# Kernel tuning notes

Measured on AMD Instinct MI355X. Metric: run time of the kernel, lower is better.

## Reference

```python
import jax, jax.numpy as jnp
import numpy as np

K_NN = 32          # configs['k']
LEAKY_ALPHA = 0.2  # configs['alpha']
NHEADS = 8         # all heads share gat_W0/gat_a0 in the weights dict -> tiled output
NEG_INF = -9e15    # masked-softmax fill used by dense GAT


@jax.custom_vjp
def grad_reverse(x):
    # GradientReversalLayer: identity forward, negated gradient backward
    return x

def _gr_fwd(x):
    return x, None

def _gr_bwd(res, g):
    return (-g,)

grad_reverse.defvjp(_gr_fwd, _gr_bwd)


def setup_inputs() -> dict:
    key = jax.random.key(0)
    ks = jax.random.split(key, 11)
    N, D = 6144, 512           # N = (num_domains+1)*batch_size = 4*1536
    H1, H2, G = 256, 128, 64   # hidden_layers=[256,128], gat_hidden=[64]
    C, ND = 16, 3              # num_classes, num source-domain discriminators

    def xav(k, shape):
        limit = np.float32(np.sqrt(6.0 / (shape[0] + shape[1])) * 1.414)
        return jax.random.uniform(k, shape, jnp.float32, -limit, limit)

    return {
        "x": jax.random.normal(ks[0], (N, D), jnp.float32),
        "fc_W0": xav(ks[1], (D, H1)),
        "fc_b0": jax.random.normal(ks[2], (H1,), jnp.float32) * 0.01,
        "fc_W1": xav(ks[3], (H1, H2)),
        "fc_b1": jax.random.normal(ks[4], (H2,), jnp.float32) * 0.01,
        "gat_W": xav(ks[5], (H2, G)),
        "gat_a": jax.random.normal(ks[6], (2 * G, 1), jnp.float32) * 0.1,
        "cls_W": xav(ks[7], (NHEADS * G, C)),
        "cls_b": jax.random.normal(ks[8], (C,), jnp.float32) * 0.01,
        "dsc_W": jax.random.uniform(ks[9], (ND, NHEADS * G, 2), jnp.float32),
        "dsc_b": jax.random.uniform(ks[10], (ND, 2), jnp.float32),
    }


def reference(x, fc_W0, fc_b0, fc_W1, fc_b1, gat_W, gat_a, cls_W, cls_b, dsc_W, dsc_b):
    # --- feature extractor MLP (Linear 'fc' + relu), dropout=0 / eval mode ---
    h = jax.nn.relu(x @ fc_W0 + fc_b0)
    h = jax.nn.relu(h @ fc_W1 + fc_b1)          # [N, 128]
    n = h.shape[0]

    # --- AdjacencyLayer / DistanceLayer: kNN over pairwise L2 distances ---
    sq = jnp.sum(h * h, axis=1)
    d2 = sq[:, None] + sq[None, :] - 2.0 * (h @ h.T)      # [N, N] squared dists
    d2 = d2 + jnp.eye(n, dtype=h.dtype) * 1e9             # exclude self from kNN
    _, idx = jax.lax.top_k(-jax.lax.stop_gradient(d2), K_NN)  # [N, K]
    adj = jnp.zeros((n, n), h.dtype).at[jnp.arange(n)[:, None], idx].set(1.0)
    adj = adj + jnp.eye(n, dtype=h.dtype)                 # self loops

    # --- dense GraphAttentionLayer (single shared head, tiled nheads times) ---
    Wh = h @ gat_W                                        # [N, G]
    Gd = Wh.shape[1]
    f1 = Wh @ gat_a[:Gd]                                  # [N, 1]
    f2 = Wh @ gat_a[Gd:]                                  # [N, 1]
    e = jax.nn.leaky_relu(f1 + f2.T, LEAKY_ALPHA)         # [N, N]
    att = jax.nn.softmax(jnp.where(adj > 0, e, NEG_INF), axis=1)
    hp = jax.nn.elu(att @ Wh)                             # [N, G]
    gat_out = jnp.tile(hp, (1, NHEADS))                   # concat of shared heads

    # --- class head + domain discriminators behind gradient reversal ---
    cls_logits = gat_out @ cls_W + cls_b                  # [N, C]
    rev = grad_reverse(gat_out)
    dsc_logits = jnp.einsum('nd,kdo->nko', rev, dsc_W) + dsc_b  # [N, ND, 2]
    return jnp.concatenate([cls_logits, dsc_logits.reshape(n, -1)], axis=1)
```

## Files before the change

kernel.cpp:

```cpp
#include <hip/hip_runtime.h>
#include <float.h>

#define N_PTS 6144
#define D_IN  512
#define H1_DIM 256
#define H2_DIM 128
#define G_DIM  64
#define KNN    32
#define NOUT   22

typedef short s8v __attribute__((ext_vector_type(8)));
typedef float f32x4 __attribute__((ext_vector_type(4)));
typedef unsigned u32x4 __attribute__((ext_vector_type(4)));
typedef unsigned short u16;
typedef unsigned long long u64;

__device__ __forceinline__ u16 f2bf(float f) {
  unsigned u = __float_as_uint(f);
  u += 0x7FFFu + ((u >> 16) & 1u);
  return (u16)(u >> 16);
}
__device__ __forceinline__ float bf2f(u16 s) {
  return __uint_as_float(((unsigned)s) << 16);
}
__device__ __forceinline__ void split3(float v, u16& a0, u16& a1, u16& a2) {
  a0 = f2bf(v);
  float r1 = v - bf2f(a0);
  a1 = f2bf(r1);
  a2 = f2bf(r1 - bf2f(a1));
}
__device__ __forceinline__ unsigned sortkey(float f) {
  unsigned ub = __float_as_uint(f);
  return (ub & 0x80000000u) ? ~ub : (ub | 0x80000000u);
}

template<int BM, bool AF32, bool SPLITK, bool BIAS, bool RELU, bool WF32, bool WSPLIT, bool WKEY, bool SYMM>
__global__ __launch_bounds__(256, 4) void mfma_gemm(
    const void* __restrict__ A0any, const u16* __restrict__ A1_, const u16* __restrict__ A2_,
    const u16* __restrict__ B0_, const u16* __restrict__ B1_, const u16* __restrict__ B2_,
    const float* __restrict__ bias,
    float* __restrict__ Cf, u16* __restrict__ C0, u16* __restrict__ C1, u16* __restrict__ C2,
    int Ktot, int Ks, int ldC, size_t MN, int rowoff)
{
  if (SYMM) {
    if ((int)(blockIdx.x >> 1) < (int)blockIdx.y) return;
  }
  const int MT = BM / 32, NT = 2;
  const int APL = BM * 32;
  const int BBASE = 3 * APL;
  __shared__ u16 lds[(BM + 64) * 32 * 3];

  const int t = threadIdx.x;
  const int lane = t & 63, wave = t >> 6;
  const int wm = wave >> 1, wn = wave & 1;
  const int m0 = blockIdx.y * BM, n0 = blockIdx.x * 64;
  const int kz = blockIdx.z * Ks;

  f32x4 acc[MT][NT] = {};

  const int pA = BM / 16;
  const int NC = 3 * pA + 12;

  for (int k0 = 0; k0 < Ks; k0 += 32) {
    if (k0) __syncthreads();
    const int kb = kz + k0;
    if (AF32) {
      const float* A = (const float*)A0any;
      #pragma unroll
      for (int c0 = 0; c0 < BM * 4; c0 += 256) {
        int c = c0 + t;
        int row = c >> 2, slot = c & 3;
        const float* g = A + (size_t)(m0 + row) * Ktot + kb + slot * 8;
        f32x4 fa = *(const f32x4*)g;
        f32x4 fb = *(const f32x4*)(g + 4);
        int dst = row * 32 + ((slot ^ ((row >> 1) & 3)) << 3);
        s8v v0, v1, v2;
        #pragma unroll
        for (int e = 0; e < 4; ++e) {
          u16 a0, a1, a2; split3(fa[e], a0, a1, a2);
          v0[e] = (short)a0; v1[e] = (short)a1; v2[e] = (short)a2;
        }
        #pragma unroll
        for (int e = 0; e < 4; ++e) {
          u16 a0, a1, a2; split3(fb[e], a0, a1, a2);
          v0[4 + e] = (short)a0; v1[4 + e] = (short)a1; v2[4 + e] = (short)a2;
        }
        *(s8v*)(lds + dst) = v0;
        *(s8v*)(lds + APL + dst) = v1;
        *(s8v*)(lds + 2 * APL + dst) = v2;
      }
      for (int c = wave; c < 12; c += 4) {
        int p = c >> 2, lc = c & 3;
        int row = lc * 16 + (lane >> 2);
        int srcslot = (lane & 3) ^ ((row >> 1) & 3);
        const u16* src = (p == 0) ? B0_ : (p == 1) ? B1_ : B2_;
        const u16* g = src + (size_t)(n0 + row) * Ktot + kb + srcslot * 8;
        __builtin_amdgcn_global_load_lds(
            (const __attribute__((address_space(1))) unsigned*)g,
            (__attribute__((address_space(3))) unsigned*)(lds + BBASE + p * 2048 + lc * 512),
            16, 0, 0);
      }
    } else {
      for (int c = wave; c < NC; c += 4) {
        const u16* src; int dstoff; int row0; int lc;
        if (c < 3 * pA) {
          int p = c / pA; lc = c % pA;
          src = (p == 0) ? (const u16*)A0any : (p == 1) ? A1_ : A2_;
          dstoff = p * APL + lc * 512;
          row0 = m0;
        } else {
          int cb = c - 3 * pA;
          int p = cb >> 2; lc = cb & 3;
          src = (p == 0) ? B0_ : (p == 1) ? B1_ : B2_;
          dstoff = BBASE + p * 2048 + lc * 512;
          row0 = n0;
        }
        int row = lc * 16 + (lane >> 2);
        int srcslot = (lane & 3) ^ ((row >> 1) & 3);
        const u16* g = src + (size_t)(row0 + row) * Ktot + kb + srcslot * 8;
        __builtin_amdgcn_global_load_lds(
            (const __attribute__((address_space(1))) unsigned*)g,
            (__attribute__((address_space(3))) unsigned*)(lds + dstoff),
            16, 0, 0);
      }
    }
    __syncthreads();

    s8v af[3][MT], bf[3][NT];
    #pragma unroll
    for (int mt = 0; mt < MT; ++mt) {
      int r = wm * (BM / 2) + mt * 16 + (lane & 15);
      int off = r * 32 + (((lane >> 4) ^ ((r >> 1) & 3)) << 3);
      #pragma unroll
      for (int p = 0; p < 3; ++p) af[p][mt] = *(const s8v*)(lds + p * APL + off);
    }
    #pragma unroll
    for (int nt = 0; nt < NT; ++nt) {
      int r = wn * 32 + nt * 16 + (lane & 15);
      int off = r * 32 + (((lane >> 4) ^ ((r >> 1) & 3)) << 3);
      #pragma unroll
      for (int p = 0; p < 3; ++p) bf[p][nt] = *(const s8v*)(lds + BBASE + p * 2048 + off);
    }
    #pragma unroll
    for (int mt = 0; mt < MT; ++mt)
      #pragma unroll
      for (int nt = 0; nt < NT; ++nt) {
        f32x4 a = acc[mt][nt];
        a = __builtin_amdgcn_mfma_f32_16x16x32_bf16(af[0][mt], bf[0][nt], a, 0, 0, 0);
        a = __builtin_amdgcn_mfma_f32_16x16x32_bf16(af[0][mt], bf[1][nt], a, 0, 0, 0);
        a = __builtin_amdgcn_mfma_f32_16x16x32_bf16(af[1][mt], bf[0][nt], a, 0, 0, 0);
        a = __builtin_amdgcn_mfma_f32_16x16x32_bf16(af[1][mt], bf[1][nt], a, 0, 0, 0);
        a = __builtin_amdgcn_mfma_f32_16x16x32_bf16(af[0][mt], bf[2][nt], a, 0, 0, 0);
        a = __builtin_amdgcn_mfma_f32_16x16x32_bf16(af[2][mt], bf[0][nt], a, 0, 0, 0);
        acc[mt][nt] = a;
      }
  }

  const bool mirror = SYMM && ((int)(blockIdx.x >> 1) > (int)blockIdx.y);
  unsigned* ldsT = (unsigned*)lds;

  #pragma unroll
  for (int mt = 0; mt < MT; ++mt) {
    #pragma unroll
    for (int nt = 0; nt < NT; ++nt) {
      int col = n0 + wn * 32 + nt * 16 + (lane & 15);
      float bv = (BIAS && !SPLITK) ? bias[col] : 0.f;
      float sqc = WKEY ? bias[col] : 0.f;
      #pragma unroll
      for (int v = 0; v < 4; ++v) {
        int row = m0 + wm * (BM / 2) + mt * 16 + (lane >> 4) * 4 + v;
        float val = acc[mt][nt][v] + bv;
        size_t o = (size_t)row * ldC + col;
        if (SPLITK) {
          Cf[(size_t)blockIdx.z * MN + o] = val;
        } else if (WKEY) {
          float f = fmaf(-2.f, val, sqc);
          unsigned uu = sortkey(f);
          if (rowoff + row == col) uu = 0xFFFFFFFFu;
          ((unsigned*)Cf)[o] = uu;
          if (mirror) {
            float fb2 = fmaf(-2.f, val, bias[row]);
            acc[mt][nt][v] = __uint_as_float(sortkey(fb2));
          }
        } else {
          if (RELU) val = fmaxf(val, 0.f);
          if (WF32) Cf[o] = val;
          if (WSPLIT) {
            u16 a0, a1, a2; split3(val, a0, a1, a2);
            C0[o] = a0; C1[o] = a1; C2[o] = a2;
          }
        }
      }
    }
  }

  if (WKEY && mirror) {
    __syncthreads();
    #pragma unroll
    for (int mt = 0; mt < MT; ++mt) {
      #pragma unroll
      for (int nt = 0; nt < NT; ++nt) {
        int cl = wn * 32 + nt * 16 + (lane & 15);
        #pragma unroll
        for (int v = 0; v < 4; ++v) {
          int rl = wm * (BM / 2) + mt * 16 + (lane >> 4) * 4 + v;
          ldsT[cl * 129 + rl] = __float_as_uint(acc[mt][nt][v]);
        }
      }
    }
    __syncthreads();
    unsigned* Cu = (unsigned*)Cf;
    for (int e = t; e < 64 * 32; e += 256) {
      int jr = e >> 5, cq = e & 31;
      u32x4 vv;
      #pragma unroll
      for (int x = 0; x < 4; ++x) vv[x] = ldsT[jr * 129 + cq * 4 + x];
      *(u32x4*)(Cu + (size_t)(n0 + jr) * ldC + m0 + cq * 4) = vv;
    }
  }
}

template<int S, bool BIAS, bool RELU, bool WF32, bool WSPLIT>
__global__ void combine(const float* __restrict__ P, const float* __restrict__ bias,
                        size_t MN, int Ncols,
                        float* __restrict__ Cf, u16* __restrict__ C0,
                        u16* __restrict__ C1, u16* __restrict__ C2)
{
  size_t idx = ((size_t)blockIdx.x * 256 + threadIdx.x) * 4;
  if (idx >= MN) return;
  f32x4 s = *(const f32x4*)(P + idx);
  #pragma unroll
  for (int z = 1; z < S; ++z) s += *(const f32x4*)(P + (size_t)z * MN + idx);
  int n = (int)(idx % (size_t)Ncols);
  #pragma unroll
  for (int e = 0; e < 4; ++e) {
    float v = s[e] + (BIAS ? bias[n + e] : 0.f);
    if (RELU) v = fmaxf(v, 0.f);
    if (WF32) Cf[idx + e] = v;
    if (WSPLIT) {
      u16 a0, a1, a2; split3(v, a0, a1, a2);
      C0[idx + e] = a0; C1[idx + e] = a1; C2[idx + e] = a2;
    }
  }
}

__global__ void prep_all(const float* __restrict__ W0, u16* __restrict__ a0,
                         u16* __restrict__ a1, u16* __restrict__ a2,
                         const float* __restrict__ W1, u16* __restrict__ b0,
                         u16* __restrict__ b1, u16* __restrict__ b2,
                         const float* __restrict__ gW, u16* __restrict__ c0,
                         u16* __restrict__ c1, u16* __restrict__ c2,
                         const float* __restrict__ cW, const float* __restrict__ cb,
                         const float* __restrict__ dW, const float* __restrict__ db,
                         float* __restrict__ Wc, float* __restrict__ bc)
{
  int id = blockIdx.x * 256 + threadIdx.x;
  const int S0 = D_IN * H1_DIM, S1 = H1_DIM * H2_DIM, S2 = H2_DIM * G_DIM;
  const int SW = S0 + S1 + S2;
  if (id < SW) {
    const float* W; u16 *p0, *p1, *p2; int K, N;
    if (id < S0)           { W = W0; p0 = a0; p1 = a1; p2 = a2; K = D_IN;   N = H1_DIM; }
    else if (id < S0 + S1) { id -= S0; W = W1; p0 = b0; p1 = b1; p2 = b2; K = H1_DIM; N = H2_DIM; }
    else                   { id -= S0 + S1; W = gW; p0 = c0; p1 = c1; p2 = c2; K = H2_DIM; N = G_DIM; }
    int k = id / N, n = id % N;
    u16 x0, x1, x2;
    split3(W[id], x0, x1, x2);
    size_t o = (size_t)n * K + k;
    p0[o] = x0; p1[o] = x1; p2[o] = x2;
    return;
  }
  id -= SW;
  if (id < 64 * NOUT) {
    int g = id / NOUT, c = id % NOUT;
    float s = 0.f;
    if (c < 16) {
      for (int r = 0; r < 8; ++r) s += cW[(r * 64 + g) * 16 + c];
    } else {
      int k = (c - 16) >> 1, o = (c - 16) & 1;
      for (int r = 0; r < 8; ++r) s += dW[k * 1024 + (r * 64 + g) * 2 + o];
    }
    Wc[id] = s;
    if (g == 0) bc[c] = (c < 16) ? cb[c] : db[c - 16];
  }
}

__global__ void row_stats(const float* __restrict__ h, const float* __restrict__ Wh,
                          const float* __restrict__ ga, float* __restrict__ sq,
                          float* __restrict__ f1, float* __restrict__ f2)
{
  int i = blockIdx.x * 256 + threadIdx.x;
  const float* hr = h + (size_t)i * H2_DIM;
  float s = 0.f;
  for (int k = 0; k < H2_DIM; ++k) { float v = hr[k]; s = fmaf(v, v, s); }
  sq[i] = s;
  const float* wr = Wh + (size_t)i * G_DIM;
  float a = 0.f, b = 0.f;
  for (int g = 0; g < G_DIM; ++g) {
    float w = wr[g];
    a = fmaf(w, ga[g], a);
    b = fmaf(w, ga[G_DIM + g], b);
  }
  f1[i] = a; f2[i] = b;
}

__global__ __launch_bounds__(256) void topk_att(const unsigned* __restrict__ Sb,
    const float* __restrict__ f1, const float* __restrict__ f2,
    const float* __restrict__ Wh, const float* __restrict__ Wc, const float* __restrict__ bc,
    float* __restrict__ out, int m0, int nrows)
{
  const int t = threadIdx.x;
  const int lane = t & 63, wv = t >> 6;
  const int row4 = (nrows - 4 - blockIdx.x * 4) + wv;
  const int i = m0 + row4;
  const unsigned* Srow = Sb + (size_t)row4 * N_PTS;

  __shared__ float WcL[64 * NOUT];
  __shared__ u64 candS[4][256];
  __shared__ int neighS[4][33];
  __shared__ float attS[4][33];
  __shared__ float hpfS[4][64];

  for (int idx = t; idx < 64 * NOUT; idx += 256) WcL[idx] = Wc[idx];
  __syncthreads();

  unsigned q[24];
  #pragma unroll
  for (int c = 0; c < 24; ++c) {
    u32x4 v = *(const u32x4*)(Srow + (c << 8) + (lane << 2));
    unsigned a = v[0] < v[1] ? v[0] : v[1];
    unsigned b = v[2] < v[3] ? v[2] : v[3];
    q[c] = a < b ? a : b;
  }

  unsigned lmin = q[0];
  #pragma unroll
  for (int c = 1; c < 24; ++c) lmin = q[c] < lmin ? q[c] : lmin;

  unsigned mnl = lmin, mxl = lmin;
  #pragma unroll
  for (int off = 32; off > 0; off >>= 1) {
    unsigned o1 = __shfl_xor(mnl, off); mnl = o1 < mnl ? o1 : mnl;
    unsigned o2 = __shfl_xor(mxl, off); mxl = o2 > mxl ? o2 : mxl;
  }

  long long lo = (long long)mnl - 1, hi = (long long)mxl;
  while (hi - lo > 1) {
    long long span = hi - lo;
    unsigned m1 = (unsigned)(lo + (span >> 2));
    unsigned m2 = (unsigned)(lo + (span >> 1));
    unsigned m3 = (unsigned)(hi - (span >> 2));
    int c1 = 0, c2 = 0, c3 = 0;
    #pragma unroll
    for (int c = 0; c < 24; ++c) {
      c1 += (q[c] <= m1);
      c2 += (q[c] <= m2);
      c3 += (q[c] <= m3);
    }
    #pragma unroll
    for (int off = 32; off > 0; off >>= 1) {
      c1 += __shfl_xor(c1, off);
      c2 += __shfl_xor(c2, off);
      c3 += __shfl_xor(c3, off);
    }
    if (c1 >= KNN)       { hi = m1; }
    else if (c2 >= KNN)  { lo = m1; hi = m2; }
    else if (c3 >= KNN)  { lo = m2; hi = m3; }
    else                 { lo = m3; }
  }
  const unsigned Q = (unsigned)hi;

  candS[wv][lane] = ~0ull;
  candS[wv][64 + lane] = ~0ull;
  candS[wv][128 + lane] = ~0ull;
  candS[wv][192 + lane] = ~0ull;
  const u64 below = (lane == 0) ? 0ull : (~0ull >> (64 - lane));
  int cnt = 0;
  #pragma unroll
  for (int c = 0; c < 24; ++c) {
    bool act = (q[c] <= Q);
    u64 mask = __ballot(act);
    if (act) {
      int pos = cnt + (int)__popcll(mask & below);
      if (pos < 64) {
        u32x4 v = *(const u32x4*)(Srow + (c << 8) + (lane << 2));
        #pragma unroll
        for (int e = 0; e < 4; ++e) {
          int j = (c << 8) + (lane << 2) + e;
          candS[wv][pos * 4 + e] = ((u64)v[e] << 13) | (unsigned)j;
        }
      }
    }
    cnt += (int)__popcll(mask);
  }

  if (cnt <= 32) {
    u64 v0 = candS[wv][2 * lane], v1 = candS[wv][2 * lane + 1];
    const int e0 = 2 * lane, e1 = e0 + 1;
    for (int k = 2; k <= 128; k <<= 1) {
      for (int j = k >> 1; j >= 2; j >>= 1) {
        int half = j >> 1;
        u64 o0 = __shfl_xor(v0, half);
        u64 o1 = __shfl_xor(v1, half);
        bool up0 = ((e0 & k) == 0) == ((e0 & j) == 0);
        bool up1 = ((e1 & k) == 0) == ((e1 & j) == 0);
        v0 = up0 ? (v0 < o0 ? v0 : o0) : (v0 > o0 ? v0 : o0);
        v1 = up1 ? (v1 < o1 ? v1 : o1) : (v1 > o1 ? v1 : o1);
      }
      bool asc = ((e0 & k) == 0);
      u64 a = v0 < v1 ? v0 : v1, b = v0 < v1 ? v1 : v0;
      v0 = asc ? a : b;
      v1 = asc ? b : a;
    }
    if (lane < 16) {
      neighS[wv][2 * lane]     = (int)(v0 & 0x1FFFu);
      neighS[wv][2 * lane + 1] = (int)(v1 & 0x1FFFu);
    }
    if (lane == 0) neighS[wv][32] = i;
  } else {
    for (int k = 2; k <= 256; k <<= 1) {
      for (int j = k >> 1; j >= 1; j >>= 1) {
        #pragma unroll
        for (int s = 0; s < 4; ++s) {
          int e = lane + s * 64;
          int p = e ^ j;
          if (p > e) {
            u64 a = candS[wv][e], b = candS[wv][p];
            bool asc = ((e & k) == 0);
            if ((a > b) == asc) { candS[wv][e] = b; candS[wv][p] = a; }
          }
        }
      }
    }
    if (lane < KNN) neighS[wv][lane] = (int)(candS[wv][lane] & 0x1FFFu);
    if (lane == 0) neighS[wv][32] = i;
  }

  {
    float e = -FLT_MAX;
    if (lane < 33) {
      float raw = f1[i] + f2[neighS[wv][lane]];
      e = raw > 0.f ? raw : 0.2f * raw;
    }
    float mx = e;
    #pragma unroll
    for (int off = 32; off > 0; off >>= 1) mx = fmaxf(mx, __shfl_xor(mx, off));
    float ex = (lane < 33) ? expf(e - mx) : 0.f;
    float sm = ex;
    #pragma unroll
    for (int off = 32; off > 0; off >>= 1) sm += __shfl_xor(sm, off);
    if (lane < 33) attS[wv][lane] = ex / sm;
  }

  {
    float s = 0.f;
    for (int m = 0; m < 33; ++m)
      s = fmaf(attS[wv][m], Wh[(size_t)neighS[wv][m] * G_DIM + lane], s);
    hpfS[wv][lane] = s > 0.f ? s : expm1f(s);
  }

  if (lane < NOUT) {
    float o = bc[lane];
    for (int g = 0; g < 64; ++g) o = fmaf(hpfS[wv][g], WcL[g * NOUT + lane], o);
    out[(size_t)i * NOUT + lane] = o;
  }
}

extern "C" void kernel_launch(void* const* d_in, const int* in_sizes, int n_in,
                              void* d_out, int out_size, void* d_ws, size_t ws_size,
                              hipStream_t stream)
{
  const float* x  = (const float*)d_in[0];
  const float* W0 = (const float*)d_in[1];
  const float* b0 = (const float*)d_in[2];
  const float* W1 = (const float*)d_in[3];
  const float* b1 = (const float*)d_in[4];
  const float* gW = (const float*)d_in[5];
  const float* ga = (const float*)d_in[6];
  const float* cW = (const float*)d_in[7];
  const float* cb = (const float*)d_in[8];
  const float* dW = (const float*)d_in[9];
  const float* db = (const float*)d_in[10];
  float* out = (float*)d_out;

  char* base = (char*)d_ws;
  char* w = base;
  auto alloc = [&](size_t bytes) { char* p = w; w += (bytes + 255) & ~(size_t)255; return p; };
  u16 *W0p[3], *W1p[3], *gWp[3], *h1p[3], *hp[3];
  for (int p = 0; p < 3; ++p) W0p[p] = (u16*)alloc((size_t)D_IN * H1_DIM * 2);
  for (int p = 0; p < 3; ++p) W1p[p] = (u16*)alloc((size_t)H1_DIM * H2_DIM * 2);
  for (int p = 0; p < 3; ++p) gWp[p] = (u16*)alloc((size_t)H2_DIM * G_DIM * 2);
  for (int p = 0; p < 3; ++p) h1p[p] = (u16*)alloc((size_t)N_PTS * H1_DIM * 2);
  for (int p = 0; p < 3; ++p) hp[p]  = (u16*)alloc((size_t)N_PTS * H2_DIM * 2);
  float* hF  = (float*)alloc((size_t)N_PTS * H2_DIM * 4);
  float* WhF = (float*)alloc((size_t)N_PTS * G_DIM * 4);
  float* sqv = (float*)alloc(N_PTS * 4);
  float* f1v = (float*)alloc(N_PTS * 4);
  float* f2v = (float*)alloc(N_PTS * 4);
  float* Wc  = (float*)alloc(64 * NOUT * 4);
  float* bc  = (float*)alloc(64 * 4);

  char* pbase = w;
  const size_t MN1 = (size_t)N_PTS * H1_DIM;
  const size_t MN2 = (size_t)N_PTS * H2_DIM;
  const size_t MN3 = (size_t)N_PTS * G_DIM;
  float* P1 = (float*)alloc(4 * MN1 * 4);
  float* P2 = (float*)alloc(4 * MN2 * 4);
  float* P3 = (float*)alloc(4 * MN3 * 4);
  float* Sb = (float*)pbase;

  size_t used_persist = (size_t)(pbase - base);
  size_t avail = (ws_size > used_persist) ? (ws_size - used_persist) / 4 : 0;
  int rowblk = 128;
  const int rcand[] = {6144, 3072, 1536, 768, 384, 256, 128};
  for (int c : rcand) { if ((size_t)c * N_PTS <= avail) { rowblk = c; break; } }

  const int TS = D_IN * H1_DIM + H1_DIM * H2_DIM + H2_DIM * G_DIM + 64 * NOUT;
  prep_all<<<(TS + 255) / 256, 256, 0, stream>>>(
      W0, W0p[0], W0p[1], W0p[2], W1, W1p[0], W1p[1], W1p[2], gW, gWp[0], gWp[1], gWp[2],
      cW, cb, dW, db, Wc, bc);

  mfma_gemm<64, true, true, false, false, false, false, false, false>
      <<<dim3(H1_DIM / 64, N_PTS / 64, 4), 256, 0, stream>>>(
      x, nullptr, nullptr, W0p[0], W0p[1], W0p[2], nullptr,
      P1, nullptr, nullptr, nullptr, D_IN, D_IN / 4, H1_DIM, MN1, 0);
  combine<4, true, true, false, true><<<(int)(MN1 / 1024), 256, 0, stream>>>(
      P1, b0, MN1, H1_DIM, nullptr, h1p[0], h1p[1], h1p[2]);

  mfma_gemm<64, false, true, false, false, false, false, false, false>
      <<<dim3(H2_DIM / 64, N_PTS / 64, 4), 256, 0, stream>>>(
      h1p[0], h1p[1], h1p[2], W1p[0], W1p[1], W1p[2], nullptr,
      P2, nullptr, nullptr, nullptr, H1_DIM, H1_DIM / 4, H2_DIM, MN2, 0);
  combine<4, true, true, true, true><<<(int)(MN2 / 1024), 256, 0, stream>>>(
      P2, b1, MN2, H2_DIM, hF, hp[0], hp[1], hp[2]);

  mfma_gemm<64, false, true, false, false, false, false, false, false>
      <<<dim3(G_DIM / 64, N_PTS / 64, 4), 256, 0, stream>>>(
      hp[0], hp[1], hp[2], gWp[0], gWp[1], gWp[2], nullptr,
      P3, nullptr, nullptr, nullptr, H2_DIM, H2_DIM / 4, G_DIM, MN3, 0);
  combine<4, false, false, true, false><<<(int)(MN3 / 1024), 256, 0, stream>>>(
      P3, nullptr, MN3, G_DIM, WhF, nullptr, nullptr, nullptr);

  row_stats<<<N_PTS / 256, 256, 0, stream>>>(hF, WhF, ga, sqv, f1v, f2v);

  if (rowblk == N_PTS) {
    mfma_gemm<128, false, false, false, false, false, false, true, true>
        <<<dim3(N_PTS / 64, N_PTS / 128, 1), 256, 0, stream>>>(
        hp[0], hp[1], hp[2], hp[0], hp[1], hp[2], sqv,
        Sb, nullptr, nullptr, nullptr, H2_DIM, H2_DIM, N_PTS, 0, 0);
    topk_att<<<N_PTS / 4, 256, 0, stream>>>((const unsigned*)Sb, f1v, f2v, WhF, Wc, bc, out, 0, N_PTS);
  } else {
    for (int b = 0; b < N_PTS / rowblk; ++b) {
      mfma_gemm<128, false, false, false, false, false, false, true, false>
          <<<dim3(N_PTS / 64, rowblk / 128, 1), 256, 0, stream>>>(
          hp[0] + (size_t)b * rowblk * H2_DIM, hp[1] + (size_t)b * rowblk * H2_DIM,
          hp[2] + (size_t)b * rowblk * H2_DIM, hp[0], hp[1], hp[2], sqv,
          Sb, nullptr, nullptr, nullptr, H2_DIM, H2_DIM, N_PTS, 0, b * rowblk);
      topk_att<<<rowblk / 4, 256, 0, stream>>>((const unsigned*)Sb, f1v, f2v, WhF, Wc, bc, out, b * rowblk, rowblk);
    }
  }
}
```

Baseline: 183.0 us.

## Store kNN distance keys as 16-bit and refine ties with exact recompute

```diff
diff --git a/kernel.cpp b/kernel.cpp
--- a/kernel.cpp
+++ b/kernel.cpp
@@ -13,6 +13,7 @@
 typedef float f32x4 __attribute__((ext_vector_type(4)));
 typedef unsigned u32x4 __attribute__((ext_vector_type(4)));
 typedef unsigned short u16;
+typedef unsigned short u16x4 __attribute__((ext_vector_type(4)));
 typedef unsigned long long u64;
 
 __device__ __forceinline__ u16 f2bf(float f) {
@@ -156,8 +157,63 @@
       }
   }
 
-  const bool mirror = SYMM && ((int)(blockIdx.x >> 1) > (int)blockIdx.y);
-  unsigned* ldsT = (unsigned*)lds;
+  if (WKEY) {
+    const bool mirror = SYMM && ((int)(blockIdx.x >> 1) > (int)blockIdx.y);
+    u16 mk[MT][NT][4];
+    __syncthreads();
+    u16* stD = lds;
+    #pragma unroll
+    for (int mt = 0; mt < MT; ++mt) {
+      #pragma unroll
+      for (int nt = 0; nt < NT; ++nt) {
+        int cl = wn * 32 + nt * 16 + (lane & 15);
+        float sqc = bias[n0 + cl];
+        #pragma unroll
+        for (int v = 0; v < 4; ++v) {
+          int rl = wm * (BM / 2) + mt * 16 + (lane >> 4) * 4 + v;
+          float val = acc[mt][nt][v];
+          float f = fmaf(-2.f, val, sqc);
+          unsigned uu = sortkey(f);
+          if (rowoff + m0 + rl == n0 + cl) uu = 0xFFFFFFFFu;
+          stD[rl * 72 + cl] = (u16)(uu >> 16);
+          if (mirror) {
+            float fm = fmaf(-2.f, val, bias[m0 + rl]);
+            mk[mt][nt][v] = (u16)(sortkey(fm) >> 16);
+          }
+        }
+      }
+    }
+    __syncthreads();
+    u16* Cu = (u16*)Cf;
+    for (int e = t; e < BM * 8; e += 256) {
+      int row = e >> 3, ch = e & 7;
+      u32x4 vv = *(const u32x4*)(stD + row * 72 + ch * 8);
+      *(u32x4*)(Cu + (size_t)(m0 + row) * ldC + n0 + ch * 8) = vv;
+    }
+    if (mirror) {
+      __syncthreads();
+      u16* stM = lds;
+      #pragma unroll
+      for (int mt = 0; mt < MT; ++mt) {
+        #pragma unroll
+        for (int nt = 0; nt < NT; ++nt) {
+          int cl = wn * 32 + nt * 16 + (lane & 15);
+          #pragma unroll
+          for (int v = 0; v < 4; ++v) {
+            int rl = wm * (BM / 2) + mt * 16 + (lane >> 4) * 4 + v;
+            stM[cl * 136 + rl] = mk[mt][nt][v];
+          }
+        }
+      }
+      __syncthreads();
+      for (int e = t; e < 64 * 16; e += 256) {
+        int row = e >> 4, ch = e & 15;
+        u32x4 vv = *(const u32x4*)(stM + row * 136 + ch * 8);
+        *(u32x4*)(Cu + (size_t)(n0 + row) * ldC + m0 + ch * 8) = vv;
+      }
+    }
+    return;
+  }
 
   #pragma unroll
   for (int mt = 0; mt < MT; ++mt) {
@@ -165,7 +221,6 @@
     for (int nt = 0; nt < NT; ++nt) {
       int col = n0 + wn * 32 + nt * 16 + (lane & 15);
       float bv = (BIAS && !SPLITK) ? bias[col] : 0.f;
-      float sqc = WKEY ? bias[col] : 0.f;
       #pragma unroll
       for (int v = 0; v < 4; ++v) {
         int row = m0 + wm * (BM / 2) + mt * 16 + (lane >> 4) * 4 + v;
@@ -173,15 +228,6 @@
         size_t o = (size_t)row * ldC + col;
         if (SPLITK) {
           Cf[(size_t)blockIdx.z * MN + o] = val;
-        } else if (WKEY) {
-          float f = fmaf(-2.f, val, sqc);
-          unsigned uu = sortkey(f);
-          if (rowoff + row == col) uu = 0xFFFFFFFFu;
-          ((unsigned*)Cf)[o] = uu;
-          if (mirror) {
-            float fb2 = fmaf(-2.f, val, bias[row]);
-            acc[mt][nt][v] = __uint_as_float(sortkey(fb2));
-          }
         } else {
           if (RELU) val = fmaxf(val, 0.f);
           if (WF32) Cf[o] = val;
@@ -191,31 +237,6 @@
           }
         }
       }
-    }
-  }
-
-  if (WKEY && mirror) {
-    __syncthreads();
-    #pragma unroll
-    for (int mt = 0; mt < MT; ++mt) {
-      #pragma unroll
-      for (int nt = 0; nt < NT; ++nt) {
-        int cl = wn * 32 + nt * 16 + (lane & 15);
-        #pragma unroll
-        for (int v = 0; v < 4; ++v) {
-          int rl = wm * (BM / 2) + mt * 16 + (lane >> 4) * 4 + v;
-          ldsT[cl * 129 + rl] = __float_as_uint(acc[mt][nt][v]);
-        }
-      }
-    }
-    __syncthreads();
-    unsigned* Cu = (unsigned*)Cf;
-    for (int e = t; e < 64 * 32; e += 256) {
-      int jr = e >> 5, cq = e & 31;
-      u32x4 vv;
-      #pragma unroll
-      for (int x = 0; x < 4; ++x) vv[x] = ldsT[jr * 129 + cq * 4 + x];
-      *(u32x4*)(Cu + (size_t)(n0 + jr) * ldC + m0 + cq * 4) = vv;
     }
   }
 }
@@ -303,19 +324,22 @@
   f1[i] = a; f2[i] = b;
 }
 
-__global__ __launch_bounds__(256) void topk_att(const unsigned* __restrict__ Sb,
+__global__ __launch_bounds__(256) void topk_att(const u16* __restrict__ Sb,
     const float* __restrict__ f1, const float* __restrict__ f2,
     const float* __restrict__ Wh, const float* __restrict__ Wc, const float* __restrict__ bc,
+    const float* __restrict__ sq, const float* __restrict__ hF,
     float* __restrict__ out, int m0, int nrows)
 {
   const int t = threadIdx.x;
   const int lane = t & 63, wv = t >> 6;
   const int row4 = (nrows - 4 - blockIdx.x * 4) + wv;
   const int i = m0 + row4;
-  const unsigned* Srow = Sb + (size_t)row4 * N_PTS;
+  const u16* Srow = Sb + (size_t)row4 * N_PTS;
 
   __shared__ float WcL[64 * NOUT];
-  __shared__ u64 candS[4][256];
+  __shared__ unsigned candS[4][384];
+  __shared__ u16 tieS[4][128];
+  __shared__ float hiL[4][128];
   __shared__ int neighS[4][33];
   __shared__ float attS[4][33];
   __shared__ float hpfS[4][64];
@@ -323,12 +347,15 @@
   for (int idx = t; idx < 64 * NOUT; idx += 256) WcL[idx] = Wc[idx];
   __syncthreads();
 
+  hiL[wv][lane]      = hF[(size_t)i * H2_DIM + lane];
+  hiL[wv][64 + lane] = hF[(size_t)i * H2_DIM + 64 + lane];
+
   unsigned q[24];
   #pragma unroll
   for (int c = 0; c < 24; ++c) {
-    u32x4 v = *(const u32x4*)(Srow + (c << 8) + (lane << 2));
-    unsigned a = v[0] < v[1] ? v[0] : v[1];
-    unsigned b = v[2] < v[3] ? v[2] : v[3];
+    u16x4 v = *(const u16x4*)(Srow + (c << 8) + (lane << 2));
+    unsigned a = v[0] < v[1] ? (unsigned)v[0] : (unsigned)v[1];
+    unsigned b = v[2] < v[3] ? (unsigned)v[2] : (unsigned)v[3];
     q[c] = a < b ? a : b;
   }
 
@@ -369,32 +396,108 @@
   }
   const unsigned Q = (unsigned)hi;
 
-  candS[wv][lane] = ~0ull;
-  candS[wv][64 + lane] = ~0ull;
-  candS[wv][128 + lane] = ~0ull;
-  candS[wv][192 + lane] = ~0ull;
+  #pragma unroll
+  for (int s = 0; s < 6; ++s) candS[wv][lane + s * 64] = 0xFFFFFFFFu;
   const u64 below = (lane == 0) ? 0ull : (~0ull >> (64 - lane));
-  int cnt = 0;
+  int qcnt = 0;
   #pragma unroll
   for (int c = 0; c < 24; ++c) {
     bool act = (q[c] <= Q);
     u64 mask = __ballot(act);
     if (act) {
-      int pos = cnt + (int)__popcll(mask & below);
-      if (pos < 64) {
-        u32x4 v = *(const u32x4*)(Srow + (c << 8) + (lane << 2));
+      int pos = qcnt + (int)__popcll(mask & below);
+      if (pos < 96) {
+        u16x4 v = *(const u16x4*)(Srow + (c << 8) + (lane << 2));
         #pragma unroll
         for (int e = 0; e < 4; ++e) {
           int j = (c << 8) + (lane << 2) + e;
-          candS[wv][pos * 4 + e] = ((u64)v[e] << 13) | (unsigned)j;
+          candS[wv][pos * 4 + e] = ((unsigned)v[e] << 13) | (unsigned)j;
         }
       }
     }
-    cnt += (int)__popcll(mask);
-  }
-
-  if (cnt <= 32) {
-    u64 v0 = candS[wv][2 * lane], v1 = candS[wv][2 * lane + 1];
+    qcnt += (int)__popcll(mask);
+  }
+
+  unsigned ck[6];
+  #pragma unroll
+  for (int s = 0; s < 6; ++s) ck[s] = candS[wv][lane + s * 64];
+
+  lo = -1; hi = 0x10000;
+  while (hi - lo > 1) {
+    long long span = hi - lo;
+    unsigned m1 = (unsigned)(lo + (span >> 2));
+    unsigned m2 = (unsigned)(lo + (span >> 1));
+    unsigned m3 = (unsigned)(hi - (span >> 2));
+    int c1 = 0, c2 = 0, c3 = 0;
+    #pragma unroll
+    for (int s = 0; s < 6; ++s) {
+      unsigned k = ck[s] >> 13;
+      c1 += (k <= m1);
+      c2 += (k <= m2);
+      c3 += (k <= m3);
+    }
+    #pragma unroll
+    for (int off = 32; off > 0; off >>= 1) {
+      c1 += __shfl_xor(c1, off);
+      c2 += __shfl_xor(c2, off);
+      c3 += __shfl_xor(c3, off);
+    }
+    if (c1 >= KNN)       { hi = m1; }
+    else if (c2 >= KNN)  { lo = m1; hi = m2; }
+    else if (c3 >= KNN)  { lo = m2; hi = m3; }
+    else                 { lo = m3; }
+  }
+  const unsigned T = (unsigned)hi;
+
+  int sA = 0, sB = 0;
+  #pragma unroll
+  for (int s = 0; s < 6; ++s) {
+    unsigned k = ck[s] >> 13;
+    bool strict = (k < T);
+    u64 ms = __ballot(strict);
+    if (strict) {
+      int pos = sA + (int)__popcll(ms & below);
+      if (pos < 32) neighS[wv][pos] = (int)(ck[s] & 0x1FFFu);
+    }
+    sA += (int)__popcll(ms);
+    bool tie = (k == T);
+    u64 mt2 = __ballot(tie);
+    if (tie) {
+      int pos = sB + (int)__popcll(mt2 & below);
+      if (pos < 128) tieS[wv][pos] = (u16)(ck[s] & 0x1FFFu);
+    }
+    sB += (int)__popcll(mt2);
+  }
+  if (sB > 128) sB = 128;
+  const int need = KNN - sA;
+
+  u64 r0 = ~0ull, r1 = ~0ull;
+  const float* hi0 = &hiL[wv][0];
+  #pragma unroll
+  for (int half = 0; half < 2; ++half) {
+    int e = lane + half * 64;
+    if (e < sB) {
+      int j = tieS[wv][e];
+      const float* hj = hF + (size_t)j * H2_DIM;
+      float dot = 0.f;
+      for (int d = 0; d < H2_DIM; d += 4) {
+        f32x4 a = *(const f32x4*)(hi0 + d);
+        f32x4 b = *(const f32x4*)(hj + d);
+        dot = fmaf(a[0], b[0], fmaf(a[1], b[1], fmaf(a[2], b[2], fmaf(a[3], b[3], dot))));
+      }
+      float f = fmaf(-2.f, dot, sq[j]);
+      u64 rk = ((u64)sortkey(f) << 13) | (unsigned)j;
+      if (half == 0) r0 = rk; else r1 = rk;
+    }
+  }
+
+  {
+    candS[wv][lane] = (unsigned)(r0 >> 32); candS[wv][64 + lane] = (unsigned)r0;
+    candS[wv][128 + lane] = (unsigned)(r1 >> 32); candS[wv][192 + lane] = (unsigned)r1;
+    u64 v0 = ((u64)candS[wv][(2 * lane) >= 64 ? 128 + (2 * lane - 64) : 2 * lane] << 32)
+           | candS[wv][(2 * lane) >= 64 ? 192 + (2 * lane - 64) : 64 + 2 * lane];
+    u64 v1 = ((u64)candS[wv][(2 * lane + 1) >= 64 ? 128 + (2 * lane + 1 - 64) : 2 * lane + 1] << 32)
+           | candS[wv][(2 * lane + 1) >= 64 ? 192 + (2 * lane + 1 - 64) : 64 + 2 * lane + 1];
     const int e0 = 2 * lane, e1 = e0 + 1;
     for (int k = 2; k <= 128; k <<= 1) {
       for (int j = k >> 1; j >= 2; j >>= 1) {
@@ -411,29 +514,10 @@
       v0 = asc ? a : b;
       v1 = asc ? b : a;
     }
-    if (lane < 16) {
-      neighS[wv][2 * lane]     = (int)(v0 & 0x1FFFu);
-      neighS[wv][2 * lane + 1] = (int)(v1 & 0x1FFFu);
-    }
-    if (lane == 0) neighS[wv][32] = i;
-  } else {
-    for (int k = 2; k <= 256; k <<= 1) {
-      for (int j = k >> 1; j >= 1; j >>= 1) {
-        #pragma unroll
-        for (int s = 0; s < 4; ++s) {
-          int e = lane + s * 64;
-          int p = e ^ j;
-          if (p > e) {
-            u64 a = candS[wv][e], b = candS[wv][p];
-            bool asc = ((e & k) == 0);
-            if ((a > b) == asc) { candS[wv][e] = b; candS[wv][p] = a; }
-          }
-        }
-      }
-    }
-    if (lane < KNN) neighS[wv][lane] = (int)(candS[wv][lane] & 0x1FFFu);
-    if (lane == 0) neighS[wv][32] = i;
-  }
+    if (e0 < need) neighS[wv][sA + e0] = (int)(v0 & 0x1FFFu);
+    if (e1 < need) neighS[wv][sA + e1] = (int)(v1 & 0x1FFFu);
+  }
+  if (lane == 0) neighS[wv][32] = i;
 
   {
     float e = -FLT_MAX;
@@ -506,13 +590,13 @@
   float* P1 = (float*)alloc(4 * MN1 * 4);
   float* P2 = (float*)alloc(4 * MN2 * 4);
   float* P3 = (float*)alloc(4 * MN3 * 4);
-  float* Sb = (float*)pbase;
+  u16* Sb = (u16*)pbase;
 
   size_t used_persist = (size_t)(pbase - base);
-  size_t avail = (ws_size > used_persist) ? (ws_size - used_persist) / 4 : 0;
+  size_t avail16 = (ws_size > used_persist) ? (ws_size - used_persist) / 2 : 0;
   int rowblk = 128;
   const int rcand[] = {6144, 3072, 1536, 768, 384, 256, 128};
-  for (int c : rcand) { if ((size_t)c * N_PTS <= avail) { rowblk = c; break; } }
+  for (int c : rcand) { if ((size_t)c * N_PTS <= avail16) { rowblk = c; break; } }
 
   const int TS = D_IN * H1_DIM + H1_DIM * H2_DIM + H2_DIM * G_DIM + 64 * NOUT;
   prep_all<<<(TS + 255) / 256, 256, 0, stream>>>(
@@ -546,16 +630,16 @@
     mfma_gemm<128, false, false, false, false, false, false, true, true>
         <<<dim3(N_PTS / 64, N_PTS / 128, 1), 256, 0, stream>>>(
         hp[0], hp[1], hp[2], hp[0], hp[1], hp[2], sqv,
-        Sb, nullptr, nullptr, nullptr, H2_DIM, H2_DIM, N_PTS, 0, 0);
-    topk_att<<<N_PTS / 4, 256, 0, stream>>>((const unsigned*)Sb, f1v, f2v, WhF, Wc, bc, out, 0, N_PTS);
+        (float*)Sb, nullptr, nullptr, nullptr, H2_DIM, H2_DIM, N_PTS, 0, 0);
+    topk_att<<<N_PTS / 4, 256, 0, stream>>>(Sb, f1v, f2v, WhF, Wc, bc, sqv, hF, out, 0, N_PTS);
   } else {
     for (int b = 0; b < N_PTS / rowblk; ++b) {
       mfma_gemm<128, false, false, false, false, false, false, true, false>
           <<<dim3(N_PTS / 64, rowblk / 128, 1), 256, 0, stream>>>(
           hp[0] + (size_t)b * rowblk * H2_DIM, hp[1] + (size_t)b * rowblk * H2_DIM,
           hp[2] + (size_t)b * rowblk * H2_DIM, hp[0], hp[1], hp[2], sqv,
-          Sb, nullptr, nullptr, nullptr, H2_DIM, H2_DIM, N_PTS, 0, b * rowblk);
-      topk_att<<<rowblk / 4, 256, 0, stream>>>((const unsigned*)Sb, f1v, f2v, WhF, Wc, bc, out, b * rowblk, rowblk);
-    }
-  }
-}
+          (float*)Sb, nullptr, nullptr, nullptr, H2_DIM, H2_DIM, N_PTS, 0, b * rowblk);
+      topk_att<<<rowblk / 4, 256, 0, stream>>>(Sb, f1v, f2v, WhF, Wc, bc, sqv, hF, out, b * rowblk, rowblk);
+    }
+  }
+}
```

Result: faster. 170.7 us (-6.7%).
